# Performance work log

Measured on AMD Instinct MI355X. Metric: run time of the kernel, lower is better.

## Reference

```python
import jax, jax.numpy as jnp
import numpy as np

B, M, K, KNN = 2, 256, 64, 16
CXYZ, CFEAT = 3, 61
CIN = CXYZ + CFEAT  # 64
MLPS = [64, 128]
SUMM = sum(MLPS)    # 192
CALIB = 64
EXP = [256, 512]
OUT = 256
EPS = 1e-5


def bn(x, g, b):
    # BatchNorm eval mode with running_mean=0, running_var=1 (channel axis 1)
    shape = (1, -1) + (1,) * (x.ndim - 2)
    return x * (g / jnp.sqrt(1.0 + EPS)).reshape(shape) + b.reshape(shape)


def knn(x, k):
    xx = jnp.sum(x * x, axis=1)                      # (B, N)
    inner = jnp.einsum('bcn,bcm->bnm', x, x)         # (B, N, N)
    pd = 2.0 * inner - xx[:, :, None] - xx[:, None, :]
    return jax.lax.top_k(pd, k)[1]                   # (B, N, k)


def graph_feature(x, idx):
    # x: (B, C, N), idx: (B, N, k) -> (B, 2C, N, k)
    xt = jnp.transpose(x, (0, 2, 1))                 # (B, N, C)
    nb = jax.vmap(lambda a, i: a[i])(xt, idx)        # (B, N, k, C)
    ctr = xt[:, :, None, :]
    feat = jnp.concatenate([nb - ctr, jnp.broadcast_to(ctr, nb.shape)], axis=-1)
    return jnp.transpose(feat, (0, 3, 1, 2))


def forward(xyz, feats, e1_w, e1_g, e1_b, e2_w, e2_g, e2_b,
            cal1_w, cal1_g, cal1_b, cal2_w, cal2_bias,
            exp1_w, exp1_g, exp1_b, exp2_w, exp2_g, exp2_b,
            red_w, red_g, red_b, sc1_w, sc1_b, sc2_w, sc2_b,
            sc_n1_g, sc_n1_b, sc_n2_g, sc_n2_b):
    x3 = xyz.reshape(B * M, K, CXYZ).transpose(0, 2, 1)      # (BM, 3, K)
    f = feats.reshape(B * M, K, CFEAT).transpose(0, 2, 1)    # (BM, 61, K)
    idx = knn(x3, KNN)                                        # USE_FEATS_DIS=False: knn once on xyz
    x = jnp.concatenate([x3, f], axis=1)                      # (BM, 64, K)
    outs = []
    for W, g, b in ((e1_w, e1_g, e1_b), (e2_w, e2_g, e2_b)):
        gf = graph_feature(x, idx)                            # (BM, 2C, K, knn)
        y = jax.nn.relu(bn(jnp.einsum('oc,bcnk->bonk', W, gf), g, b))
        x = y.max(axis=-1)                                    # (BM, mlp_i, K)
        outs.append(x)
    x = jnp.concatenate(outs, axis=1)                         # (BM, 192, K)
    c = jax.nn.relu(bn(jnp.einsum('oc,bcn->bon', cal1_w, x), cal1_g, cal1_b))
    c = jnp.einsum('oc,bcn->bon', cal2_w, c) + cal2_bias[None, :, None]
    x = jax.nn.sigmoid(c) * x
    x = jax.nn.relu(bn(jnp.einsum('oc,bcn->bon', exp1_w, x), exp1_g, exp1_b))
    x = jax.nn.relu(bn(jnp.einsum('oc,bcn->bon', exp2_w, x), exp2_g, exp2_b))
    x = x.max(axis=-1).reshape(B, M, EXP[1]).transpose(0, 2, 1)  # (B, 512, M)
    x = jax.nn.relu(bn(jnp.einsum('oc,bcm->bom', red_w, x), red_g, red_b))
    x = bn(x + x, sc_n1_g, sc_n1_b)
    h = jax.nn.relu(jnp.einsum('oc,bcm->bom', sc1_w, x) + sc1_b[None, :, None])
    h = jnp.einsum('oc,bcm->bom', sc2_w, h) + sc2_b[None, :, None]
    x = bn(x + h, sc_n2_g, sc_n2_b)
    return x                                                  # (B, 256, M)


def setup_inputs() -> dict:
    key = jax.random.key(0)
    ks = jax.random.split(key, 16)
    w = lambda k, s: jax.random.normal(k, s, jnp.float32) * 0.05
    ones = lambda n: jnp.ones((n,), jnp.float32)
    zeros = lambda n: jnp.zeros((n,), jnp.float32)
    return {
        'xyz': jax.random.normal(ks[0], (B, M, K, CXYZ), jnp.float32),
        'feats': jax.random.normal(ks[1], (B, M, K, CFEAT), jnp.float32),
        'e1_w': w(ks[2], (MLPS[0], 2 * CIN)), 'e1_g': ones(MLPS[0]), 'e1_b': zeros(MLPS[0]),
        'e2_w': w(ks[3], (MLPS[1], 2 * MLPS[0])), 'e2_g': ones(MLPS[1]), 'e2_b': zeros(MLPS[1]),
        'cal1_w': w(ks[4], (CALIB, SUMM)), 'cal1_g': ones(CALIB), 'cal1_b': zeros(CALIB),
        'cal2_w': w(ks[5], (SUMM, CALIB)), 'cal2_bias': zeros(SUMM),
        'exp1_w': w(ks[6], (EXP[0], SUMM)), 'exp1_g': ones(EXP[0]), 'exp1_b': zeros(EXP[0]),
        'exp2_w': w(ks[7], (EXP[1], EXP[0])), 'exp2_g': ones(EXP[1]), 'exp2_b': zeros(EXP[1]),
        'red_w': w(ks[8], (OUT, EXP[1])), 'red_g': ones(OUT), 'red_b': zeros(OUT),
        'sc1_w': w(ks[9], (OUT, OUT)), 'sc1_b': zeros(OUT),
        'sc2_w': w(ks[10], (OUT, OUT)), 'sc2_b': zeros(OUT),
        'sc_n1_g': ones(OUT), 'sc_n1_b': zeros(OUT),
        'sc_n2_g': ones(OUT), 'sc_n2_b': zeros(OUT),
    }


def reference(xyz, feats, e1_w, e1_g, e1_b, e2_w, e2_g, e2_b,
              cal1_w, cal1_g, cal1_b, cal2_w, cal2_bias,
              exp1_w, exp1_g, exp1_b, exp2_w, exp2_g, exp2_b,
              red_w, red_g, red_b, sc1_w, sc1_b, sc2_w, sc2_b,
              sc_n1_g, sc_n1_b, sc_n2_g, sc_n2_b):
    return forward(xyz, feats, e1_w, e1_g, e1_b, e2_w, e2_g, e2_b,
                   cal1_w, cal1_g, cal1_b, cal2_w, cal2_bias,
                   exp1_w, exp1_g, exp1_b, exp2_w, exp2_g, exp2_b,
                   red_w, red_g, red_b, sc1_w, sc1_b, sc2_w, sc2_b,
                   sc_n1_g, sc_n1_b, sc_n2_g, sc_n2_b)
```

## Files before the change

kernel.cpp:

```cpp
#include <hip/hip_runtime.h>
#include <hip/hip_bf16.h>
#include <math.h>
#include <stddef.h>

#define DEV __device__ __forceinline__
__device__ const float BNS = 0.99999500003749968f;

typedef __bf16 bf16x8 __attribute__((ext_vector_type(8)));
typedef float  f32x4  __attribute__((ext_vector_type(4)));

#define MF(a,b,c) __builtin_amdgcn_mfma_f32_16x16x32_bf16(a,b,c,0,0,0)

DEV unsigned short f2bs(float v){
  union{ __hip_bfloat16 b; unsigned short u; } c; c.b=__float2bfloat16(v); return c.u;
}
DEV float bs2f(unsigned short u){
  union{ unsigned short u; __hip_bfloat16 b; } c; c.u=u; return __bfloat162float(c.b);
}

DEV void put_split4(unsigned short* chunks, int n, int c0, const float* v){
  int cc=c0>>5, u=(c0>>3)&3, e=c0&7;
  unsigned short* base = chunks + cc*4096;
  unsigned short h0=f2bs(v[0]), h1=f2bs(v[1]), h2=f2bs(v[2]), h3=f2bs(v[3]);
  ushort4 hq = make_ushort4(h0,h1,h2,h3);
  ushort4 lq = make_ushort4(f2bs(v[0]-bs2f(h0)), f2bs(v[1]-bs2f(h1)),
                            f2bs(v[2]-bs2f(h2)), f2bs(v[3]-bs2f(h3)));
  *(ushort4*)&base[(n*8 + (u     ^ (n&7)))*8 + e] = hq;
  *(ushort4*)&base[(n*8 + ((u+4) ^ (n&7)))*8 + e] = lq;
}
DEV void get_split4(const unsigned short* chunks, int n, int c0, float* v){
  int cc=c0>>5, u=(c0>>3)&3, e=c0&7;
  const unsigned short* base = chunks + cc*4096;
  ushort4 hq = *(const ushort4*)&base[(n*8 + (u     ^ (n&7)))*8 + e];
  ushort4 lq = *(const ushort4*)&base[(n*8 + ((u+4) ^ (n&7)))*8 + e];
  v[0]=bs2f(hq.x)+bs2f(lq.x); v[1]=bs2f(hq.y)+bs2f(lq.y);
  v[2]=bs2f(hq.z)+bs2f(lq.z); v[3]=bs2f(hq.w)+bs2f(lq.w);
}


__global__ __launch_bounds__(256) void k_prep(const float* __restrict__ e1_w,
    const float* __restrict__ e2_w, const float* __restrict__ cal1_w,
    const float* __restrict__ cal2_w, const float* __restrict__ exp1_w,
    const float* __restrict__ exp2_w, unsigned short* __restrict__ Whi,
    unsigned short* __restrict__ Wlo,
    const float* __restrict__ red_w, const float* __restrict__ sc1_w,
    const float* __restrict__ sc2_w, float* __restrict__ Wt_red,
    float* __restrict__ Wt_s1, float* __restrict__ Wt_s2){
  __shared__ float s[32][33];
  int bid = blockIdx.x;
  if(bid < 896){
    const float* src; unsigned short *hi,*lo; int mode, O=0, i0;
    if(bid<32)      { src=e1_w;  hi=Whi;       lo=Wlo;       mode=1; O= 64; i0=bid*256; }
    else if(bid<96) { src=e2_w;  hi=Whi+8192;  lo=Wlo+8192;  mode=1; O=128; i0=(bid-32)*256; }
    else if(bid<144){ src=cal1_w;hi=Whi+24576; lo=Wlo+24576; mode=0;        i0=(bid-96)*256; }
    else if(bid<192){ src=cal2_w;hi=Whi+36864; lo=Wlo+36864; mode=0;        i0=(bid-144)*256; }
    else if(bid<384){ src=exp1_w;hi=Whi+49152; lo=Wlo+49152; mode=0;        i0=(bid-192)*256; }
    else            { src=exp2_w;hi=Whi+98304; lo=Wlo+98304; mode=0;        i0=(bid-384)*256; }
    int i = i0 + threadIdx.x;
    float v;
    if(mode==0) v = src[i];
    else {
      int row=i>>6, c=i&63;
      v = (row<O) ? src[row*128+c] : (src[(row-O)*128+64+c]-src[(row-O)*128+c]);
    }
    unsigned short h=f2bs(v); hi[i]=h; lo[i]=f2bs(v-bs2f(h));
  } else {
    int lb = bid-896;
    const float* in; float* out; int O,K;
    if(lb<128){ in=red_w; out=Wt_red; O=256; K=512; }
    else if(lb<192){ in=sc1_w; out=Wt_s1; O=256; K=256; lb-=128; }
    else { in=sc2_w; out=Wt_s2; O=256; K=256; lb-=192; }
    int nt=O>>5;
    int to=lb%nt, tk=lb/nt;
    int c=threadIdx.x&31, r8=threadIdx.x>>5;
    #pragma unroll
    for(int p=0;p<4;p++){
      int r=r8+p*8;
      s[r][c]=in[(size_t)(to*32+r)*K + tk*32 + c];
    }
    __syncthreads();
    #pragma unroll
    for(int p=0;p<4;p++){
      int r=r8+p*8;
      out[(size_t)(tk*32+r)*O + to*32 + c]=s[c][r];
    }
  }
}

__global__ __launch_bounds__(512) void k_knne12(const float* __restrict__ xyz,
    const float* __restrict__ feats,
    const unsigned short* __restrict__ W1h, const unsigned short* __restrict__ W1l,
    const unsigned short* __restrict__ W2h, const unsigned short* __restrict__ W2l,
    const float* __restrict__ g1, const float* __restrict__ b1,
    const float* __restrict__ g2, const float* __restrict__ b2,
    unsigned short* __restrict__ cat){
  __shared__ float bufA[64*65];
  __shared__ float bufB[64*65];
  __shared__ __align__(16) unsigned short sb[64*136];
  __shared__ int   ips[64*16];
  __shared__ float sx0[64], sx1[64], sx2[64], sxx[64];
  int bm = blockIdx.x;
  int tid = threadIdx.x, n = tid&63, s = tid>>6;
  int wid = tid>>6, lane = tid&63;
  int l15 = lane&15, q = lane>>4;
  if(s==0){
    const float* xp = xyz + (size_t)(bm*64+n)*3;
    float px=xp[0], py=xp[1], pz=xp[2];
    sx0[n]=px; sx1[n]=py; sx2[n]=pz; sxx[n]=px*px+py*py+pz*pz;
  }
  __syncthreads();
  {
    int p = lane>>3, seg = lane&7;
    int n1 = wid*8 + p;
    float px=sx0[n1], py=sx1[n1], pz=sx2[n1], xxn=sxx[n1];
    float pdr[8];
    #pragma unroll
    for(int t=0;t<8;t++){
      int m = seg*8+t;
      pdr[t] = 2.f*(px*sx0[m]+py*sx1[m]+pz*sx2[m]) - xxn - sxx[m];
    }
    for(int j=0;j<16;j++){
      float bv=-3.4e38f; int bi=seg*8;
      #pragma unroll
      for(int t=0;t<8;t++){ if(pdr[t]>bv){bv=pdr[t]; bi=seg*8+t;} }
      float ov; int oi;
      ov=__shfl_xor(bv,1); oi=__shfl_xor(bi,1);
      if(ov>bv || (ov==bv && oi<bi)){bv=ov;bi=oi;}
      ov=__shfl_xor(bv,2); oi=__shfl_xor(bi,2);
      if(ov>bv || (ov==bv && oi<bi)){bv=ov;bi=oi;}
      ov=__shfl_xor(bv,4); oi=__shfl_xor(bi,4);
      if(ov>bv || (ov==bv && oi<bi)){bv=ov;bi=oi;}
      if(seg==0) ips[n1*16+j]=bi;
      if((bi>>3)==seg) pdr[bi&7]=-3.4e38f;
    }
  }
  {
    if(s==0){
      unsigned short* r = sb + n*136;
      float px=sx0[n], py=sx1[n], pz=sx2[n];
      unsigned short h;
      h=f2bs(px); r[0]=h; r[64]=f2bs(px-bs2f(h));
      h=f2bs(py); r[1]=h; r[65]=f2bs(py-bs2f(h));
      h=f2bs(pz); r[2]=h; r[66]=f2bs(pz-bs2f(h));
    }
    const float* fb = feats + (size_t)bm*64*61;
    #pragma unroll
    for(int i=0;i<8;i++){
      int idx = tid + i*512;
      if(idx<3904){
        float v = fb[idx];
        int row = idx/61, cc = idx - row*61;
        unsigned short h=f2bs(v);
        sb[row*136 + 3+cc]      = h;
        sb[row*136 + 64 + 3+cc] = f2bs(v-bs2f(h));
      }
    }
  }
  __syncthreads();
  {
    int rbase = wid*16;
    f32x4 acc[4];
    #pragma unroll
    for(int d=0;d<4;d++) acc[d]=(f32x4){0.f,0.f,0.f,0.f};
    #pragma unroll
    for(int kc=0;kc<2;kc++){
      int k0=kc*32;
      size_t a0=(size_t)(rbase+l15)*64 + k0 + q*8;
      bf16x8 a0h=*(const bf16x8*)(W1h+a0), a0l=*(const bf16x8*)(W1l+a0);
      #pragma unroll
      for(int nt=0;nt<4;nt++){
        int row = nt*16 + l15;
        bf16x8 bh = *(const bf16x8*)&sb[row*136 + k0 + q*8];
        bf16x8 bl = *(const bf16x8*)&sb[row*136 + 64 + k0 + q*8];
        acc[nt]=MF(a0h,bh,acc[nt]);
        acc[nt]=MF(a0h,bl,acc[nt]);
        acc[nt]=MF(a0l,bh,acc[nt]);
      }
    }
    __syncthreads();
    float* dst = (wid<4)? bufA : bufB;
    int ro = (wid&3)*16;
    #pragma unroll
    for(int nt=0;nt<4;nt++)
      #pragma unroll
      for(int rr=0;rr<4;rr++)
        dst[(ro+q*4+rr)*65 + nt*16+l15] = acc[nt][rr];
  }
  __syncthreads();
  {
    int o = lane;
    float sc = g1[o]*BNS, bi = b1[o];
    #pragma unroll 4
    for(int j=0;j<8;j++){
      int nn = wid*8 + j;
      const int* ip = &ips[nn*16];
      float mz = -3.4e38f;
      #pragma unroll
      for(int k=0;k<16;k++) mz = fmaxf(mz, bufA[o*65 + ip[k]]);
      float v = fmaxf(sc*(mz + bufB[o*65 + nn]) + bi, 0.f);
      unsigned short hv = f2bs(v), lv = f2bs(v - bs2f(hv));
      size_t cb = ((size_t)bm*64+nn)*384 + o;
      cat[cb] = hv; cat[cb+192] = lv;
      sb[nn*136 + o] = hv; sb[nn*136 + 64 + o] = lv;
    }
  }
  for(int ch=0; ch<2; ch++){
    __syncthreads();
    int wrow = ((wid<4)?0:128) + ch*64 + (wid&3)*16;
    f32x4 acc[4];
    #pragma unroll
    for(int d=0;d<4;d++) acc[d]=(f32x4){0.f,0.f,0.f,0.f};
    #pragma unroll
    for(int kc=0;kc<2;kc++){
      int k0=kc*32;
      size_t a0=(size_t)(wrow+l15)*64 + k0 + q*8;
      bf16x8 a0h=*(const bf16x8*)(W2h+a0), a0l=*(const bf16x8*)(W2l+a0);
      #pragma unroll
      for(int nt=0;nt<4;nt++){
        int row = nt*16 + l15;
        bf16x8 bh = *(const bf16x8*)&sb[row*136 + k0 + q*8];
        bf16x8 bl = *(const bf16x8*)&sb[row*136 + 64 + k0 + q*8];
        acc[nt]=MF(a0h,bh,acc[nt]);
        acc[nt]=MF(a0h,bl,acc[nt]);
        acc[nt]=MF(a0l,bh,acc[nt]);
      }
    }
    __syncthreads();
    float* dst = (wid<4)? bufA : bufB;
    int ro = (wid&3)*16;
    #pragma unroll
    for(int nt=0;nt<4;nt++)
      #pragma unroll
      for(int rr=0;rr<4;rr++)
        dst[(ro+q*4+rr)*65 + nt*16+l15] = acc[nt][rr];
    __syncthreads();
    int o = ch*64 + lane;
    float sc = g2[o]*BNS, bi = b2[o];
    #pragma unroll 4
    for(int j=0;j<8;j++){
      int nn = wid*8 + j;
      const int* ip = &ips[nn*16];
      float mz = -3.4e38f;
      #pragma unroll
      for(int k=0;k<16;k++) mz = fmaxf(mz, bufA[lane*65 + ip[k]]);
      float v = fmaxf(sc*(mz + bufB[lane*65 + nn]) + bi, 0.f);
      unsigned short hv = f2bs(v);
      size_t cb = ((size_t)bm*64+nn)*384 + 64 + o;
      cat[cb] = hv; cat[cb+192] = f2bs(v - bs2f(hv));
    }
  }
}

__global__ __launch_bounds__(512,4) void k_mlp(
    const unsigned short* __restrict__ Whi, const unsigned short* __restrict__ Wlo,
    const unsigned short* __restrict__ cats,
    const float* __restrict__ c1g, const float* __restrict__ c1b,
    const float* __restrict__ c2bias,
    const float* __restrict__ e1g, const float* __restrict__ e1b,
    const float* __restrict__ e2g, const float* __restrict__ e2b,
    float* __restrict__ pool){
  __shared__ __align__(16) unsigned short buf[8*4096];
  __shared__ __align__(16) unsigned short calB[2*4096];
  int bm = blockIdx.x;
  int tid = threadIdx.x, wid = tid>>6, lane = tid&63;
  int l15 = lane&15, q = lane>>4;

  const unsigned short* w1h = Whi + 24576;
  const unsigned short* w1l = Wlo + 24576;
  int c1ot = wid>>1, c1rh = wid&1;
  size_t c1wo0 = (size_t)(c1ot*16+l15)*192 + q*8;
  bf16x8 cah = *(const bf16x8*)(w1h+c1wo0);
  bf16x8 cal_ = *(const bf16x8*)(w1l+c1wo0);

  size_t xb = (size_t)bm*24576;
  #pragma unroll
  for(int i=0;i<6;i++){
    int U = tid + i*512;
    int kc = U>>9, w = U&511, rr = w>>3, up = w&7, u = up ^ (rr&7);
    const unsigned short* src = cats + xb + (size_t)rr*384
      + (u<4 ? (kc*32 + u*8) : (192 + kc*32 + (u-4)*8));
    *(uint4*)&buf[kc*4096 + w*8] = *(const uint4*)src;
  }
  __syncthreads();

  f32x4 a0={0.f,0.f,0.f,0.f}, a1={0.f,0.f,0.f,0.f};
  {
    int r0 = c1rh*32+l15, r1 = c1rh*32+16+l15;
    __builtin_amdgcn_s_setprio(1);
    #pragma unroll
    for(int kc=0;kc<6;kc++){
      bf16x8 nah, nal;
      if(kc<5){
        size_t wo = c1wo0 + (kc+1)*32;
        nah=*(const bf16x8*)(w1h+wo); nal=*(const bf16x8*)(w1l+wo);
      }
      const unsigned short* cb = buf + kc*4096;
      bf16x8 xh0=*(const bf16x8*)&cb[(r0*8+((  q)^(r0&7)))*8];
      bf16x8 xl0=*(const bf16x8*)&cb[(r0*8+((4+q)^(r0&7)))*8];
      bf16x8 xh1=*(const bf16x8*)&cb[(r1*8+((  q)^(r1&7)))*8];
      bf16x8 xl1=*(const bf16x8*)&cb[(r1*8+((4+q)^(r1&7)))*8];
      a0=MF(cah,xh0,a0); a1=MF(cah,xh1,a1);
      a0=MF(cah,xl0,a0); a1=MF(cah,xl1,a1);
      a0=MF(cal_,xh0,a0); a1=MF(cal_,xh1,a1);
      cah=nah; cal_=nal;
    }
    __builtin_amdgcn_s_setprio(0);
  }
  const unsigned short* w2h = Whi + 36864;
  const unsigned short* w2l = Wlo + 36864;
  bf16x8 c2h[6], c2l[6];
  #pragma unroll
  for(int i=0;i<6;i++){
    int ot = (wid*6+i)>>2;
    size_t wo=(size_t)(ot*16+l15)*64 + q*8;
    c2h[i]=*(const bf16x8*)(w2h+wo); c2l[i]=*(const bf16x8*)(w2l+wo);
  }
  {
    int c0 = c1ot*16+q*4;
    float4 sg = *(const float4*)&c1g[c0];
    float4 bb = *(const float4*)&c1b[c0];
    float v0[4], v1[4];
    v0[0]=fmaxf(a0[0]*sg.x*BNS+bb.x,0.f); v1[0]=fmaxf(a1[0]*sg.x*BNS+bb.x,0.f);
    v0[1]=fmaxf(a0[1]*sg.y*BNS+bb.y,0.f); v1[1]=fmaxf(a1[1]*sg.y*BNS+bb.y,0.f);
    v0[2]=fmaxf(a0[2]*sg.z*BNS+bb.z,0.f); v1[2]=fmaxf(a1[2]*sg.z*BNS+bb.z,0.f);
    v0[3]=fmaxf(a0[3]*sg.w*BNS+bb.w,0.f); v1[3]=fmaxf(a1[3]*sg.w*BNS+bb.w,0.f);
    put_split4(calB, c1rh*32+l15,    c0, v0);
    put_split4(calB, c1rh*32+16+l15, c0, v1);
  }
  __syncthreads();
  f32x4 ac[6];
  #pragma unroll
  for(int i=0;i<6;i++) ac[i]=(f32x4){0.f,0.f,0.f,0.f};
  #pragma unroll
  for(int kc=0;kc<2;kc++){
    const unsigned short* cb = calB + kc*4096;
    if(kc==1){
      #pragma unroll
      for(int i=0;i<6;i++){
        int ot = (wid*6+i)>>2;
        size_t wo=(size_t)(ot*16+l15)*64 + 32 + q*8;
        c2h[i]=*(const bf16x8*)(w2h+wo); c2l[i]=*(const bf16x8*)(w2l+wo);
      }
    }
    __builtin_amdgcn_s_setprio(1);
    #pragma unroll
    for(int i=0;i<6;i++){
      int nf=(wid*6+i)&3;
      int r=nf*16+l15;
      bf16x8 xh=*(const bf16x8*)&cb[(r*8+((  q)^(r&7)))*8];
      bf16x8 xl=*(const bf16x8*)&cb[(r*8+((4+q)^(r&7)))*8];
      ac[i]=MF(c2h[i],xh,ac[i]); ac[i]=MF(c2h[i],xl,ac[i]); ac[i]=MF(c2l[i],xh,ac[i]);
    }
    __builtin_amdgcn_s_setprio(0);
  }
  const unsigned short* e1wh=Whi+49152; const unsigned short* e1wl=Wlo+49152;
  int ob1 = wid*32;
  bf16x8 p1h[2], p1l[2];
  #pragma unroll
  for(int mt=0;mt<2;mt++){
    size_t wo=(size_t)(ob1+mt*16+l15)*192 + q*8;
    p1h[mt]=*(const bf16x8*)(e1wh+wo); p1l[mt]=*(const bf16x8*)(e1wl+wo);
  }
  #pragma unroll
  for(int i=0;i<6;i++){
    int j=wid*6+i, ot=j>>2, nf=j&3, n=nf*16+l15;
    int c0=ot*16+q*4;
    float4 cb4 = *(const float4*)&c2bias[c0];
    float xv[4];
    get_split4(buf, n, c0, xv);
    xv[0] *= 1.f/(1.f+__expf(-(ac[i][0]+cb4.x)));
    xv[1] *= 1.f/(1.f+__expf(-(ac[i][1]+cb4.y)));
    xv[2] *= 1.f/(1.f+__expf(-(ac[i][2]+cb4.z)));
    xv[3] *= 1.f/(1.f+__expf(-(ac[i][3]+cb4.w)));
    put_split4(buf, n, c0, xv);
  }
  __syncthreads();
  {
    f32x4 e1a[2][4];
    #pragma unroll
    for(int a=0;a<2;a++)
      #pragma unroll
      for(int d=0;d<4;d++) e1a[a][d]=(f32x4){0.f,0.f,0.f,0.f};
    __builtin_amdgcn_s_setprio(1);
    #pragma unroll
    for(int kc=0;kc<6;kc++){
      bf16x8 nh[2], nl[2];
      if(kc<5){
        #pragma unroll
        for(int mt=0;mt<2;mt++){
          size_t wo=(size_t)(ob1+mt*16+l15)*192 + (kc+1)*32 + q*8;
          nh[mt]=*(const bf16x8*)(e1wh+wo); nl[mt]=*(const bf16x8*)(e1wl+wo);
        }
      }
      const unsigned short* cb = buf + kc*4096;
      #pragma unroll
      for(int nf=0;nf<4;nf++){
        int r=nf*16+l15;
        bf16x8 xh=*(const bf16x8*)&cb[(r*8+((  q)^(r&7)))*8];
        bf16x8 xl=*(const bf16x8*)&cb[(r*8+((4+q)^(r&7)))*8];
        e1a[0][nf]=MF(p1h[0],xh,e1a[0][nf]); e1a[1][nf]=MF(p1h[1],xh,e1a[1][nf]);
        e1a[0][nf]=MF(p1h[0],xl,e1a[0][nf]); e1a[1][nf]=MF(p1h[1],xl,e1a[1][nf]);
        e1a[0][nf]=MF(p1l[0],xh,e1a[0][nf]); e1a[1][nf]=MF(p1l[1],xh,e1a[1][nf]);
      }
      p1h[0]=nh[0]; p1h[1]=nh[1]; p1l[0]=nl[0]; p1l[1]=nl[1];
    }
    __builtin_amdgcn_s_setprio(0);
    __syncthreads();
    const unsigned short* e2wh=Whi+98304; const unsigned short* e2wl=Wlo+98304;
    int ob2 = wid*64;
    bf16x8 p2h[4], p2l[4];
    #pragma unroll
    for(int mt=0;mt<4;mt++){
      size_t wo=(size_t)(ob2+mt*16+l15)*256 + q*8;
      p2h[mt]=*(const bf16x8*)(e2wh+wo); p2l[mt]=*(const bf16x8*)(e2wl+wo);
    }
    #pragma unroll
    for(int mt=0;mt<2;mt++){
      int c0 = ob1+mt*16+q*4;
      float4 sg = *(const float4*)&e1g[c0];
      float4 bb = *(const float4*)&e1b[c0];
      #pragma unroll
      for(int nf=0;nf<4;nf++){
        float v[4];
        v[0]=fmaxf(e1a[mt][nf][0]*sg.x*BNS+bb.x,0.f);
        v[1]=fmaxf(e1a[mt][nf][1]*sg.y*BNS+bb.y,0.f);
        v[2]=fmaxf(e1a[mt][nf][2]*sg.z*BNS+bb.z,0.f);
        v[3]=fmaxf(e1a[mt][nf][3]*sg.w*BNS+bb.w,0.f);
        put_split4(buf, nf*16+l15, c0, v);
      }
    }
    __syncthreads();
    f32x4 a2[4][4];
    #pragma unroll
    for(int a=0;a<4;a++)
      #pragma unroll
      for(int d=0;d<4;d++) a2[a][d]=(f32x4){0.f,0.f,0.f,0.f};
    {
      const unsigned short* cb = buf;
      __builtin_amdgcn_s_setprio(1);
      #pragma unroll
      for(int nf=0;nf<4;nf++){
        int r=nf*16+l15;
        bf16x8 xh=*(const bf16x8*)&cb[(r*8+((  q)^(r&7)))*8];
        bf16x8 xl=*(const bf16x8*)&cb[(r*8+((4+q)^(r&7)))*8];
        #pragma unroll
        for(int mt=0;mt<4;mt++) a2[mt][nf]=MF(p2h[mt],xh,a2[mt][nf]);
        #pragma unroll
        for(int mt=0;mt<4;mt++) a2[mt][nf]=MF(p2h[mt],xl,a2[mt][nf]);
        #pragma unroll
        for(int mt=0;mt<4;mt++) a2[mt][nf]=MF(p2l[mt],xh,a2[mt][nf]);
      }
      __builtin_amdgcn_s_setprio(0);
    }
    for(int kc=1;kc<8;kc++){
      bf16x8 ch[4], cl[4];
      #pragma unroll
      for(int mt=0;mt<4;mt++){
        size_t wo=(size_t)(ob2+mt*16+l15)*256 + kc*32 + q*8;
        ch[mt]=*(const bf16x8*)(e2wh+wo); cl[mt]=*(const bf16x8*)(e2wl+wo);
      }
      const unsigned short* cb = buf + kc*4096;
      __builtin_amdgcn_s_setprio(1);
      #pragma unroll
      for(int nf=0;nf<4;nf++){
        int r=nf*16+l15;
        bf16x8 xh=*(const bf16x8*)&cb[(r*8+((  q)^(r&7)))*8];
        bf16x8 xl=*(const bf16x8*)&cb[(r*8+((4+q)^(r&7)))*8];
        #pragma unroll
        for(int mt=0;mt<4;mt++) a2[mt][nf]=MF(ch[mt],xh,a2[mt][nf]);
        #pragma unroll
        for(int mt=0;mt<4;mt++) a2[mt][nf]=MF(ch[mt],xl,a2[mt][nf]);
      }
      #pragma unroll
      for(int nf=0;nf<4;nf++){
        int r=nf*16+l15;
        bf16x8 xh=*(const bf16x8*)&cb[(r*8+((  q)^(r&7)))*8];
        #pragma unroll
        for(int mt=0;mt<4;mt++) a2[mt][nf]=MF(cl[mt],xh,a2[mt][nf]);
      }
      __builtin_amdgcn_s_setprio(0);
    }
    int b = bm>>8, m = bm&255;
    #pragma unroll
    for(int mt=0;mt<4;mt++){
      int c0 = ob2+mt*16+q*4;
      float4 sg = *(const float4*)&e2g[c0];
      float4 bb = *(const float4*)&e2b[c0];
      float s[4]={sg.x*BNS,sg.y*BNS,sg.z*BNS,sg.w*BNS};
      float bbv[4]={bb.x,bb.y,bb.z,bb.w};
      #pragma unroll
      for(int rr=0;rr<4;rr++){
        float v = a2[mt][0][rr]*s[rr]+bbv[rr];
        v = fmaxf(v, a2[mt][1][rr]*s[rr]+bbv[rr]);
        v = fmaxf(v, a2[mt][2][rr]*s[rr]+bbv[rr]);
        v = fmaxf(v, a2[mt][3][rr]*s[rr]+bbv[rr]);
        v = fmaxf(v, 0.f);
        v = fmaxf(v, __shfl_xor(v,1));
        v = fmaxf(v, __shfl_xor(v,2));
        v = fmaxf(v, __shfl_xor(v,4));
        v = fmaxf(v, __shfl_xor(v,8));
        if(l15==0) pool[((size_t)b*512 + c0+rr)*256 + m] = v;
      }
    }
  }
}

__global__ __launch_bounds__(1024) void k_headf(const float* __restrict__ Wt_red,
    const float* __restrict__ Wt_s1, const float* __restrict__ Wt_s2,
    const float* __restrict__ pool, float* __restrict__ Og,
    const float* __restrict__ red_g, const float* __restrict__ red_b,
    const float* __restrict__ n1g, const float* __restrict__ n1b,
    const float* __restrict__ s1b, const float* __restrict__ s2b,
    const float* __restrict__ n2g, const float* __restrict__ n2b){
  __shared__ float P[512*3];
  __shared__ float X1[256*3];
  __shared__ float H[256*3];
  __shared__ float PB[256*9];
  int g = blockIdx.x;
  int b = g>>7, mg = g&127;
  int m0 = mg*2;
  int tid = threadIdx.x;
  int o = tid&255, h = tid>>8;
  if(tid<512){
    int c = tid;
    float2 v = *(const float2*)&pool[((size_t)b*512+c)*256 + m0];
    P[c*3+0]=v.x; P[c*3+1]=v.y;
  }
  __syncthreads();
  float a0=0.f, a1=0.f;
  {
    int c0 = h*128;
    #pragma unroll 8
    for(int i=0;i<128;i++){
      int c = c0+i;
      float w = Wt_red[c*256+o];
      a0 += w*P[c*3]; a1 += w*P[c*3+1];
    }
  }
  PB[o*9+h*2]=a0; PB[o*9+h*2+1]=a1;
  __syncthreads();
  a0 = (PB[o*9+0]+PB[o*9+2])+(PB[o*9+4]+PB[o*9+6]);
  a1 = (PB[o*9+1]+PB[o*9+3])+(PB[o*9+5]+PB[o*9+7]);
  float x0r,x1r;
  {
    float s=red_g[o]*BNS, bi=red_b[o], s1=n1g[o]*BNS, b1=n1b[o];
    float r0=fmaxf(a0*s+bi,0.f), r1=fmaxf(a1*s+bi,0.f);
    x0r=2.f*r0*s1+b1; x1r=2.f*r1*s1+b1;
    if(h==0){ X1[o*3]=x0r; X1[o*3+1]=x1r; }
  }
  __syncthreads();
  a0=0.f; a1=0.f;
  {
    int c0 = h*64;
    #pragma unroll 8
    for(int i=0;i<64;i++){
      int c = c0+i;
      float w = Wt_s1[c*256+o];
      a0 += w*X1[c*3]; a1 += w*X1[c*3+1];
    }
  }
  PB[o*9+h*2]=a0; PB[o*9+h*2+1]=a1;
  __syncthreads();
  a0 = (PB[o*9+0]+PB[o*9+2])+(PB[o*9+4]+PB[o*9+6]);
  a1 = (PB[o*9+1]+PB[o*9+3])+(PB[o*9+5]+PB[o*9+7]);
  {
    float bi=s1b[o];
    if(h==0){ H[o*3]=fmaxf(a0+bi,0.f); H[o*3+1]=fmaxf(a1+bi,0.f); }
  }
  __syncthreads();
  a0=0.f; a1=0.f;
  {
    int c0 = h*64;
    #pragma unroll 8
    for(int i=0;i<64;i++){
      int c = c0+i;
      float w = Wt_s2[c*256+o];
      a0 += w*H[c*3]; a1 += w*H[c*3+1];
    }
  }
  PB[o*9+h*2]=a0; PB[o*9+h*2+1]=a1;
  __syncthreads();
  if(h==0){
    a0 = (PB[o*9+0]+PB[o*9+2])+(PB[o*9+4]+PB[o*9+6]);
    a1 = (PB[o*9+1]+PB[o*9+3])+(PB[o*9+5]+PB[o*9+7]);
    float bi=s2b[o], s2=n2g[o]*BNS, b2=n2b[o];
    float v0=(x0r+a0+bi)*s2+b2, v1=(x1r+a1+bi)*s2+b2;
    *(float2*)&Og[((size_t)b*256+o)*256 + m0] = make_float2(v0,v1);
  }
}

extern "C" void kernel_launch(void* const* d_in, const int* in_sizes, int n_in,
                              void* d_out, int out_size, void* d_ws, size_t ws_size,
                              hipStream_t stream){
  const float* xyz     =(const float*)d_in[0];
  const float* feats   =(const float*)d_in[1];
  const float* e1_w    =(const float*)d_in[2];
  const float* e1_g    =(const float*)d_in[3];
  const float* e1_b    =(const float*)d_in[4];
  const float* e2_w    =(const float*)d_in[5];
  const float* e2_g    =(const float*)d_in[6];
  const float* e2_b    =(const float*)d_in[7];
  const float* cal1_w  =(const float*)d_in[8];
  const float* cal1_g  =(const float*)d_in[9];
  const float* cal1_b  =(const float*)d_in[10];
  const float* cal2_w  =(const float*)d_in[11];
  const float* cal2_bias=(const float*)d_in[12];
  const float* exp1_w  =(const float*)d_in[13];
  const float* exp1_g  =(const float*)d_in[14];
  const float* exp1_b  =(const float*)d_in[15];
  const float* exp2_w  =(const float*)d_in[16];
  const float* exp2_g  =(const float*)d_in[17];
  const float* exp2_b  =(const float*)d_in[18];
  const float* red_w   =(const float*)d_in[19];
  const float* red_g   =(const float*)d_in[20];
  const float* red_b   =(const float*)d_in[21];
  const float* sc1_w   =(const float*)d_in[22];
  const float* sc1_b   =(const float*)d_in[23];
  const float* sc2_w   =(const float*)d_in[24];
  const float* sc2_b   =(const float*)d_in[25];
  const float* sc_n1_g =(const float*)d_in[26];
  const float* sc_n1_b =(const float*)d_in[27];
  const float* sc_n2_g =(const float*)d_in[28];
  const float* sc_n2_b =(const float*)d_in[29];

  char* wsb=(char*)d_ws;
  unsigned short* cats=(unsigned short*)(wsb + 10485760);
  float*          pool=(float*)         (wsb + 69206016);
  unsigned short* Whi =(unsigned short*)(wsb + 75497472);
  unsigned short* Wlo =(unsigned short*)(wsb + 76021760);
  float*          Wt_red=(float*)       (wsb + 76546048);
  float*          Wt_s1 =(float*)       (wsb + 77070336);
  float*          Wt_s2 =(float*)       (wsb + 77332480);
  unsigned short* e1e_h=Whi;          unsigned short* e1e_l=Wlo;
  unsigned short* e2e_h=Whi+8192;     unsigned short* e2e_l=Wlo+8192;

  k_prep      <<<1152,256,0,stream>>>(e1_w,e2_w,cal1_w,cal2_w,exp1_w,exp2_w,Whi,Wlo,
                                      red_w,sc1_w,sc2_w,Wt_red,Wt_s1,Wt_s2);
  k_knne12    <<<512,512,0,stream>>>(xyz,feats,e1e_h,e1e_l,e2e_h,e2e_l,
                                     e1_g,e1_b,e2_g,e2_b,cats);
  k_mlp       <<<512,512,0,stream>>>(Whi,Wlo,cats,cal1_g,cal1_b,cal2_bias,
                                     exp1_g,exp1_b,exp2_g,exp2_b,pool);
  k_headf     <<<256,1024,0,stream>>>(Wt_red,Wt_s1,Wt_s2,pool,(float*)d_out,
                                      red_g,red_b,sc_n1_g,sc_n1_b,sc1_b,sc2_b,sc_n2_g,sc_n2_b);
}
```

Measured before the change: 237.4 us.

## Coarsen weight prep blocks, prefetch feats early, drop MFMA priority hints

The weight-conversion kernel now has each block handle 1024 elements for the plain-copy matrices, which cuts the grid from 1152 to 552 blocks. The knn/edge-conv kernel issues its global loads of the feature tile at kernel start into registers, so their latency overlaps the knn top-k phase. All s_setprio raise/lower pairs around the MFMA loops in the MLP kernel are removed. These are three unrelated tweaks: fewer launched blocks, load-latency hiding at the cost of 8 more registers per thread, and a change to wave scheduling priority.

```diff
diff --git a/kernel.cpp b/kernel.cpp
--- a/kernel.cpp
+++ b/kernel.cpp
@@ -48,24 +48,28 @@
     float* __restrict__ Wt_s1, float* __restrict__ Wt_s2){
   __shared__ float s[32][33];
   int bid = blockIdx.x;
-  if(bid < 896){
-    const float* src; unsigned short *hi,*lo; int mode, O=0, i0;
-    if(bid<32)      { src=e1_w;  hi=Whi;       lo=Wlo;       mode=1; O= 64; i0=bid*256; }
-    else if(bid<96) { src=e2_w;  hi=Whi+8192;  lo=Wlo+8192;  mode=1; O=128; i0=(bid-32)*256; }
-    else if(bid<144){ src=cal1_w;hi=Whi+24576; lo=Wlo+24576; mode=0;        i0=(bid-96)*256; }
-    else if(bid<192){ src=cal2_w;hi=Whi+36864; lo=Wlo+36864; mode=0;        i0=(bid-144)*256; }
-    else if(bid<384){ src=exp1_w;hi=Whi+49152; lo=Wlo+49152; mode=0;        i0=(bid-192)*256; }
-    else            { src=exp2_w;hi=Whi+98304; lo=Wlo+98304; mode=0;        i0=(bid-384)*256; }
+  if(bid < 96){
+    const float* src; unsigned short *hi,*lo; int O, i0;
+    if(bid<32){ src=e1_w; hi=Whi;      lo=Wlo;      O= 64; i0=bid*256; }
+    else      { src=e2_w; hi=Whi+8192; lo=Wlo+8192; O=128; i0=(bid-32)*256; }
     int i = i0 + threadIdx.x;
-    float v;
-    if(mode==0) v = src[i];
-    else {
-      int row=i>>6, c=i&63;
-      v = (row<O) ? src[row*128+c] : (src[(row-O)*128+64+c]-src[(row-O)*128+c]);
-    }
+    int row=i>>6, c=i&63;
+    float v = (row<O) ? src[row*128+c] : (src[(row-O)*128+64+c]-src[(row-O)*128+c]);
     unsigned short h=f2bs(v); hi[i]=h; lo[i]=f2bs(v-bs2f(h));
+  } else if(bid < 296){
+    const float* src; unsigned short *hi,*lo; int i0;
+    if(bid<108)      { src=cal1_w; hi=Whi+24576; lo=Wlo+24576; i0=(bid-96)*1024; }
+    else if(bid<120) { src=cal2_w; hi=Whi+36864; lo=Wlo+36864; i0=(bid-108)*1024; }
+    else if(bid<168) { src=exp1_w; hi=Whi+49152; lo=Wlo+49152; i0=(bid-120)*1024; }
+    else             { src=exp2_w; hi=Whi+98304; lo=Wlo+98304; i0=(bid-168)*1024; }
+    #pragma unroll
+    for(int p=0;p<4;p++){
+      int i = i0 + p*256 + threadIdx.x;
+      float v = src[i];
+      unsigned short h=f2bs(v); hi[i]=h; lo[i]=f2bs(v-bs2f(h));
+    }
   } else {
-    int lb = bid-896;
+    int lb = bid-296;
     const float* in; float* out; int O,K;
     if(lb<128){ in=red_w; out=Wt_red; O=256; K=512; }
     else if(lb<192){ in=sc1_w; out=Wt_s1; O=256; K=256; lb-=128; }
@@ -103,6 +107,13 @@
   int tid = threadIdx.x, n = tid&63, s = tid>>6;
   int wid = tid>>6, lane = tid&63;
   int l15 = lane&15, q = lane>>4;
+  const float* fb = feats + (size_t)bm*3904;
+  float fv[8];
+  #pragma unroll
+  for(int i=0;i<8;i++){
+    int idx = tid + i*512;
+    fv[i] = (idx<3904) ? fb[idx] : 0.f;
+  }
   if(s==0){
     const float* xp = xyz + (size_t)(bm*64+n)*3;
     float px=xp[0], py=xp[1], pz=xp[2];
@@ -143,12 +154,11 @@
       h=f2bs(py); r[1]=h; r[65]=f2bs(py-bs2f(h));
       h=f2bs(pz); r[2]=h; r[66]=f2bs(pz-bs2f(h));
     }
-    const float* fb = feats + (size_t)bm*64*61;
     #pragma unroll
     for(int i=0;i<8;i++){
       int idx = tid + i*512;
       if(idx<3904){
-        float v = fb[idx];
+        float v = fv[i];
         int row = idx/61, cc = idx - row*61;
         unsigned short h=f2bs(v);
         sb[row*136 + 3+cc]      = h;
@@ -286,7 +296,6 @@
   f32x4 a0={0.f,0.f,0.f,0.f}, a1={0.f,0.f,0.f,0.f};
   {
     int r0 = c1rh*32+l15, r1 = c1rh*32+16+l15;
-    __builtin_amdgcn_s_setprio(1);
     #pragma unroll
     for(int kc=0;kc<6;kc++){
       bf16x8 nah, nal;
@@ -304,7 +313,6 @@
       a0=MF(cal_,xh0,a0); a1=MF(cal_,xh1,a1);
       cah=nah; cal_=nal;
     }
-    __builtin_amdgcn_s_setprio(0);
   }
   const unsigned short* w2h = Whi + 36864;
   const unsigned short* w2l = Wlo + 36864;
@@ -342,7 +350,6 @@
         c2h[i]=*(const bf16x8*)(w2h+wo); c2l[i]=*(const bf16x8*)(w2l+wo);
       }
     }
-    __builtin_amdgcn_s_setprio(1);
     #pragma unroll
     for(int i=0;i<6;i++){
       int nf=(wid*6+i)&3;
@@ -351,7 +358,6 @@
       bf16x8 xl=*(const bf16x8*)&cb[(r*8+((4+q)^(r&7)))*8];
       ac[i]=MF(c2h[i],xh,ac[i]); ac[i]=MF(c2h[i],xl,ac[i]); ac[i]=MF(c2l[i],xh,ac[i]);
     }
-    __builtin_amdgcn_s_setprio(0);
   }
   const unsigned short* e1wh=Whi+49152; const unsigned short* e1wl=Wlo+49152;
   int ob1 = wid*32;
@@ -381,7 +387,6 @@
     for(int a=0;a<2;a++)
       #pragma unroll
       for(int d=0;d<4;d++) e1a[a][d]=(f32x4){0.f,0.f,0.f,0.f};
-    __builtin_amdgcn_s_setprio(1);
     #pragma unroll
     for(int kc=0;kc<6;kc++){
       bf16x8 nh[2], nl[2];
@@ -404,7 +409,6 @@
       }
       p1h[0]=nh[0]; p1h[1]=nh[1]; p1l[0]=nl[0]; p1l[1]=nl[1];
     }
-    __builtin_amdgcn_s_setprio(0);
     __syncthreads();
     const unsigned short* e2wh=Whi+98304; const unsigned short* e2wl=Wlo+98304;
     int ob2 = wid*64;
@@ -437,7 +441,6 @@
       for(int d=0;d<4;d++) a2[a][d]=(f32x4){0.f,0.f,0.f,0.f};
     {
       const unsigned short* cb = buf;
-      __builtin_amdgcn_s_setprio(1);
       #pragma unroll
       for(int nf=0;nf<4;nf++){
         int r=nf*16+l15;
@@ -450,7 +453,6 @@
         #pragma unroll
         for(int mt=0;mt<4;mt++) a2[mt][nf]=MF(p2l[mt],xh,a2[mt][nf]);
       }
-      __builtin_amdgcn_s_setprio(0);
     }
     for(int kc=1;kc<8;kc++){
       bf16x8 ch[4], cl[4];
@@ -460,7 +462,6 @@
         ch[mt]=*(const bf16x8*)(e2wh+wo); cl[mt]=*(const bf16x8*)(e2wl+wo);
       }
       const unsigned short* cb = buf + kc*4096;
-      __builtin_amdgcn_s_setprio(1);
       #pragma unroll
       for(int nf=0;nf<4;nf++){
         int r=nf*16+l15;
@@ -478,7 +479,6 @@
         #pragma unroll
         for(int mt=0;mt<4;mt++) a2[mt][nf]=MF(cl[mt],xh,a2[mt][nf]);
       }
-      __builtin_amdgcn_s_setprio(0);
     }
     int b = bm>>8, m = bm&255;
     #pragma unroll
@@ -634,8 +634,8 @@
   unsigned short* e1e_h=Whi;          unsigned short* e1e_l=Wlo;
   unsigned short* e2e_h=Whi+8192;     unsigned short* e2e_l=Wlo+8192;
 
-  k_prep      <<<1152,256,0,stream>>>(e1_w,e2_w,cal1_w,cal2_w,exp1_w,exp2_w,Whi,Wlo,
-                                      red_w,sc1_w,sc2_w,Wt_red,Wt_s1,Wt_s2);
+  k_prep      <<<552,256,0,stream>>>(e1_w,e2_w,cal1_w,cal2_w,exp1_w,exp2_w,Whi,Wlo,
+                                     red_w,sc1_w,sc2_w,Wt_red,Wt_s1,Wt_s2);
   k_knne12    <<<512,512,0,stream>>>(xyz,feats,e1e_h,e1e_l,e2e_h,e2e_l,
                                      e1_g,e1_b,e2_g,e2_b,cats);
   k_mlp       <<<512,512,0,stream>>>(Whi,Wlo,cats,cal1_g,cal1_b,cal2_bias,
```

New measurement: 236.9 us. No clear change (-0.2%).
